# Performance work log

Hardware: AMD Instinct MI355X
Metric: run time of the kernel (lower is better)

Reference implementation:

```python
import jax, jax.numpy as jnp
import numpy as np

N, C, H, W = 512, 2048, 16, 8
NUM_CLASSES = 751
ALPHA = 1.2      # margin
LAMB = 0.5       # self.l
SIGMA = 0.8      # osm_sigma
BN_EPS = 1e-5


def setup_inputs() -> dict:
    key = jax.random.key(0)
    k1, k2, k3 = jax.random.split(key, 3)
    features = jax.random.normal(k1, (N, C, H, W), dtype=jnp.float32)
    targets = jax.random.randint(k2, (N,), 0, NUM_CLASSES)
    gamma = jnp.ones((C,), dtype=jnp.float32)  # BN weight, init 1 (weights_init_kaiming)
    # kaiming_uniform_(a=sqrt(5)) on [NUM_CLASSES, C]: bound = 1/sqrt(C)
    bound = 1.0 / np.sqrt(C)
    weight = jax.random.uniform(k3, (NUM_CLASSES, C), jnp.float32, -bound, bound)
    return {"features": features, "targets": targets, "gamma": gamma, "weight": weight}


def _l2norm(x, axis=-1):
    return x / jnp.maximum(jnp.linalg.norm(x, axis=axis, keepdims=True), 1e-12)


def reference(features, targets, gamma, weight):
    n = features.shape[0]
    # AdaptiveAvgPool2d(1) + Flatten
    global_feat = jnp.mean(features, axis=(2, 3))  # [n, C]
    # NoBiasBatchNorm1d (training mode: batch stats, biased var, no bias)
    mu = jnp.mean(global_feat, axis=0)
    var = jnp.var(global_feat, axis=0)
    bn_feat = (global_feat - mu) / jnp.sqrt(var + BN_EPS) * gamma
    bn_feat = _l2norm(bn_feat, axis=1)  # F.normalize

    # pairwise euclidean distance
    sq = jnp.sum(bn_feat * bn_feat, axis=1)                       # [n]
    dist2 = sq[:, None] + sq[None, :] - 2.0 * (bn_feat @ bn_feat.T)
    dist = jnp.sqrt(jnp.clip(dist2, 1e-12, None))                 # [n, n]

    S_pos = jnp.exp(-(dist * dist) / (SIGMA * SIGMA))
    S_neg = jnp.clip(ALPHA - dist, 1e-12, None)
    p_mask = targets[:, None] == targets[None, :]                 # [n, n] bool
    S = jnp.where(p_mask, S_pos, S_neg)

    # per-sample attention: exp(logits)[i, t_i] / sum_j exp(logits)[i, j] == softmax
    logits = bn_feat @ _l2norm(weight, axis=1).T                  # [n, num_classes]
    probs = jax.nn.softmax(logits, axis=1)
    atten = probs[jnp.arange(n), targets]                         # [n]
    A = jnp.minimum(atten[None, :], atten[:, None])               # [n, n]

    Wmat = S * A
    off_diag = 1.0 - jnp.eye(n, dtype=Wmat.dtype)
    W_P = Wmat * p_mask.astype(Wmat.dtype) * off_diag
    W_N = Wmat * (~p_mask).astype(Wmat.dtype) * off_diag

    L_P = 0.5 * jnp.sum(W_P * dist * dist) / jnp.sum(W_P)
    L_N = 0.5 * jnp.sum(W_N * S_neg * S_neg) / jnp.sum(W_N)
    L = (1.0 - LAMB) * L_P + LAMB * L_N
    return (L, global_feat)
```

## Files before the change

kernel.cpp:

```cpp
#include <hip/hip_runtime.h>
#include <hip/hip_bf16.h>
#include <math.h>

#define N_S   512
#define C_S   2048
#define HW_S  128
#define NCLS  751
#define NCLSP 768
#define ALPHA 1.2f
#define LAMB  0.5f
#define SIGMA 0.8f
#define BN_EPS 1e-5f

typedef __attribute__((ext_vector_type(8))) short short8;
typedef __attribute__((ext_vector_type(4))) float f32x4;

__device__ __forceinline__ unsigned short f2bf(float x) {
    __hip_bfloat16 h = __float2bfloat16(x);
    return *reinterpret_cast<unsigned short*>(&h);
}

__global__ void init_accum_kernel(float* __restrict__ accum) {
    if (threadIdx.x < 4) accum[threadIdx.x] = 0.0f;
}

__global__ __launch_bounds__(256) void pool_kernel(const float* __restrict__ feat,
                                                   float* __restrict__ gf,
                                                   float* __restrict__ out_gf) {
    int tid  = blockIdx.x * 256 + threadIdx.x;
    int pair = tid >> 5;
    int lane = tid & 31;
    const float4* p = reinterpret_cast<const float4*>(feat + (size_t)pair * HW_S);
    float4 v = p[lane];
    float s = v.x + v.y + v.z + v.w;
    #pragma unroll
    for (int off = 16; off > 0; off >>= 1) s += __shfl_down(s, off, 32);
    if (lane == 0) {
        float m = s * (1.0f / HW_S);
        gf[pair]     = m;
        out_gf[pair] = m;
    }
}

__global__ __launch_bounds__(256) void meanvar_kernel(const float* __restrict__ gf,
                                                      const float* __restrict__ gamma,
                                                      float* __restrict__ mu_out,
                                                      float* __restrict__ scale_out) {
    int c = blockIdx.x * 256 + threadIdx.x;
    float sum = 0.f, sumsq = 0.f;
    for (int n = 0; n < N_S; ++n) {
        float x = gf[(size_t)n * C_S + c];
        sum += x; sumsq += x * x;
    }
    float mu  = sum * (1.0f / N_S);
    float var = sumsq * (1.0f / N_S) - mu * mu;
    mu_out[c]    = mu;
    scale_out[c] = gamma[c] / sqrtf(var + BN_EPS);
}

__global__ __launch_bounds__(256) void bnnorm_kernel(const float* __restrict__ gf,
                                                     const float* __restrict__ mu,
                                                     const float* __restrict__ scale,
                                                     unsigned short* __restrict__ bnnh,
                                                     float* __restrict__ sq) {
    int n = blockIdx.x, t = threadIdx.x;
    const float* row = gf + (size_t)n * C_S;
    float v[8];
    float ss = 0.f;
    #pragma unroll
    for (int k = 0; k < 8; ++k) {
        int c = t + k * 256;
        float x = (row[c] - mu[c]) * scale[c];
        v[k] = x; ss += x * x;
    }
    __shared__ float red[4];
    __shared__ float sinv;
    #pragma unroll
    for (int off = 32; off > 0; off >>= 1) ss += __shfl_down(ss, off, 64);
    if ((t & 63) == 0) red[t >> 6] = ss;
    __syncthreads();
    if (t == 0) {
        float tot = red[0] + red[1] + red[2] + red[3];
        float inv = 1.0f / fmaxf(sqrtf(tot), 1e-12f);
        sinv  = inv;
        sq[n] = tot * inv * inv;
    }
    __syncthreads();
    float inv = sinv;
    unsigned short* orow = bnnh + (size_t)n * C_S;
    #pragma unroll
    for (int k = 0; k < 8; ++k) orow[t + k * 256] = f2bf(v[k] * inv);
}

__global__ __launch_bounds__(256) void wnorm_kernel(const float* __restrict__ w,
                                                    unsigned short* __restrict__ wnh) {
    int kcls = blockIdx.x, t = threadIdx.x;
    unsigned short* orow = wnh + (size_t)kcls * C_S;
    if (kcls >= NCLS) {
        #pragma unroll
        for (int k = 0; k < 8; ++k) orow[t + k * 256] = 0;
        return;
    }
    const float* row = w + (size_t)kcls * C_S;
    float v[8];
    float ss = 0.f;
    #pragma unroll
    for (int k = 0; k < 8; ++k) {
        float x = row[t + k * 256];
        v[k] = x; ss += x * x;
    }
    __shared__ float red[4];
    __shared__ float sinv;
    #pragma unroll
    for (int off = 32; off > 0; off >>= 1) ss += __shfl_down(ss, off, 64);
    if ((t & 63) == 0) red[t >> 6] = ss;
    __syncthreads();
    if (t == 0) sinv = 1.0f / fmaxf(sqrtf(red[0] + red[1] + red[2] + red[3]), 1e-12f);
    __syncthreads();
    float inv = sinv;
    #pragma unroll
    for (int k = 0; k < 8; ++k) orow[t + k * 256] = f2bf(v[k] * inv);
}

__global__ __launch_bounds__(256) void mfma_gemm_nt(const unsigned short* __restrict__ Ah,
                                                    const unsigned short* __restrict__ Bh,
                                                    float* __restrict__ Cm,
                                                    int K, int ldc) {
    int wave = threadIdx.x >> 6;
    int lane = threadIdx.x & 63;
    int m0 = blockIdx.x * 64 + wave * 16;
    int n0 = blockIdx.y * 64;
    int mrow = m0 + (lane & 15);
    int kq   = (lane >> 4) * 8;
    f32x4 acc0 = {0.f,0.f,0.f,0.f}, acc1 = {0.f,0.f,0.f,0.f};
    f32x4 acc2 = {0.f,0.f,0.f,0.f}, acc3 = {0.f,0.f,0.f,0.f};
    const unsigned short* arow = Ah + (size_t)mrow * K + kq;
    const unsigned short* brow = Bh + (size_t)(n0 + (lane & 15)) * K + kq;
    for (int k = 0; k < K; k += 32) {
        short8 a  = *reinterpret_cast<const short8*>(arow + k);
        short8 b0 = *reinterpret_cast<const short8*>(brow + k);
        short8 b1 = *reinterpret_cast<const short8*>(brow + 16 * K + k);
        short8 b2 = *reinterpret_cast<const short8*>(brow + 32 * K + k);
        short8 b3 = *reinterpret_cast<const short8*>(brow + 48 * K + k);
        acc0 = __builtin_amdgcn_mfma_f32_16x16x32_bf16(a, b0, acc0, 0, 0, 0);
        acc1 = __builtin_amdgcn_mfma_f32_16x16x32_bf16(a, b1, acc1, 0, 0, 0);
        acc2 = __builtin_amdgcn_mfma_f32_16x16x32_bf16(a, b2, acc2, 0, 0, 0);
        acc3 = __builtin_amdgcn_mfma_f32_16x16x32_bf16(a, b3, acc3, 0, 0, 0);
    }
    int ccol  = lane & 15;
    int crow0 = m0 + (lane >> 4) * 4;
    #pragma unroll
    for (int r = 0; r < 4; ++r) {
        float* orow = Cm + (size_t)(crow0 + r) * ldc + n0 + ccol;
        orow[0]  = acc0[r];
        orow[16] = acc1[r];
        orow[32] = acc2[r];
        orow[48] = acc3[r];
    }
}

__global__ __launch_bounds__(256) void softmax_atten_kernel(const float* __restrict__ logits,
                                                            const int* __restrict__ targets,
                                                            float* __restrict__ atten) {
    int n = blockIdx.x, t = threadIdx.x;
    const float* row = logits + (size_t)n * NCLSP;
    __shared__ float red[4];
    __shared__ float srmax, srsum;
    float m = -1e30f;
    for (int k = t; k < NCLS; k += 256) m = fmaxf(m, row[k]);
    #pragma unroll
    for (int off = 32; off > 0; off >>= 1) m = fmaxf(m, __shfl_down(m, off, 64));
    if ((t & 63) == 0) red[t >> 6] = m;
    __syncthreads();
    if (t == 0) srmax = fmaxf(fmaxf(red[0], red[1]), fmaxf(red[2], red[3]));
    __syncthreads();
    float rm = srmax;
    float s = 0.f;
    for (int k = t; k < NCLS; k += 256) s += expf(row[k] - rm);
    #pragma unroll
    for (int off = 32; off > 0; off >>= 1) s += __shfl_down(s, off, 64);
    if ((t & 63) == 0) red[t >> 6] = s;
    __syncthreads();
    if (t == 0) {
        srsum = red[0] + red[1] + red[2] + red[3];
        atten[n] = expf(row[targets[n]] - rm) / srsum;
    }
}

__global__ __launch_bounds__(256) void pair_reduce_kernel(const float* __restrict__ G,
                                                          const float* __restrict__ sq,
                                                          const float* __restrict__ atten,
                                                          const int* __restrict__ targets,
                                                          float* __restrict__ accum) {
    float numP = 0.f, denP = 0.f, numN = 0.f, denN = 0.f;
    const float inv_sig2 = 1.0f / (SIGMA * SIGMA);
    for (int p = blockIdx.x * 256 + threadIdx.x; p < N_S * N_S; p += 256 * 256) {
        int i = p >> 9, j = p & (N_S - 1);
        if (i == j) continue;
        float d2   = fmaxf(sq[i] + sq[j] - 2.0f * G[p], 1e-12f);
        float dist = sqrtf(d2);
        float sneg = fmaxf(ALPHA - dist, 1e-12f);
        float Aij  = fminf(atten[i], atten[j]);
        if (targets[i] == targets[j]) {
            float Wm = expf(-d2 * inv_sig2) * Aij;
            numP += Wm * d2; denP += Wm;
        } else {
            float Wm = sneg * Aij;
            numN += Wm * sneg * sneg; denN += Wm;
        }
    }
    #pragma unroll
    for (int off = 32; off > 0; off >>= 1) {
        numP += __shfl_down(numP, off, 64);
        denP += __shfl_down(denP, off, 64);
        numN += __shfl_down(numN, off, 64);
        denN += __shfl_down(denN, off, 64);
    }
    __shared__ float red[4][4];
    int t = threadIdx.x;
    if ((t & 63) == 0) {
        int w = t >> 6;
        red[w][0] = numP; red[w][1] = denP; red[w][2] = numN; red[w][3] = denN;
    }
    __syncthreads();
    if (t < 4) {
        float s = red[0][t] + red[1][t] + red[2][t] + red[3][t];
        atomicAdd(&accum[t], s);
    }
}

__global__ void finalize_kernel(const float* __restrict__ accum, float* __restrict__ out) {
    float L_P = 0.5f * accum[0] / accum[1];
    float L_N = 0.5f * accum[2] / accum[3];
    out[0] = (1.0f - LAMB) * L_P + LAMB * L_N;
}

extern "C" void kernel_launch(void* const* d_in, const int* in_sizes, int n_in,
                              void* d_out, int out_size, void* d_ws, size_t ws_size,
                              hipStream_t stream) {
    const float* features = (const float*)d_in[0];
    const int*   targets  = (const int*)d_in[1];
    const float* gamma    = (const float*)d_in[2];
    const float* weight   = (const float*)d_in[3];
    float* out = (float*)d_out;

    float* ws     = (float*)d_ws;
    float* gf     = ws;
    float* mu     = gf + 1048576;
    float* scale  = mu + 2048;
    float* sq     = scale + 2048;
    float* atten  = sq + 512;
    float* accum  = atten + 512;
    float* logits = accum + 8;
    float* G      = logits + 393216;
    unsigned short* bnnh = (unsigned short*)(G + 262144);
    unsigned short* wnh  = bnnh + 1048576;

    hipLaunchKernelGGL(init_accum_kernel, dim3(1), dim3(64), 0, stream, accum);
    hipLaunchKernelGGL(pool_kernel, dim3((N_S * C_S) / 8), dim3(256), 0, stream,
                       features, gf, out + 1);
    hipLaunchKernelGGL(meanvar_kernel, dim3(C_S / 256), dim3(256), 0, stream,
                       gf, gamma, mu, scale);
    hipLaunchKernelGGL(bnnorm_kernel, dim3(N_S), dim3(256), 0, stream,
                       gf, mu, scale, bnnh, sq);
    hipLaunchKernelGGL(wnorm_kernel, dim3(NCLSP), dim3(256), 0, stream, weight, wnh);
    hipLaunchKernelGGL(mfma_gemm_nt, dim3(N_S / 64, NCLSP / 64), dim3(256), 0, stream,
                       bnnh, wnh, logits, C_S, NCLSP);
    hipLaunchKernelGGL(softmax_atten_kernel, dim3(N_S), dim3(256), 0, stream,
                       logits, targets, atten);
    hipLaunchKernelGGL(mfma_gemm_nt, dim3(N_S / 64, N_S / 64), dim3(256), 0, stream,
                       bnnh, bnnh, G, C_S, N_S);
    hipLaunchKernelGGL(pair_reduce_kernel, dim3(256), dim3(256), 0, stream,
                       G, sq, atten, targets, accum);
    hipLaunchKernelGGL(finalize_kernel, dim3(1), dim3(1), 0, stream, accum, out);
}
```

Baseline: 787.1 us.

## Restructure pooling, column stats, GEMM grid and fold init/finalize kernels

The pool kernel now handles 16 pairs per block with two float4 loads per lane, zeroes the accumulators itself, and writes pooled features straight into the output buffer, which removes the extra gf copy. meanvar now splits the 512 rows across 8 thread groups per column with a shared-memory reduction, so many more blocks run. The GEMM becomes one wave per block over 16-row tiles, which multiplies the block count for better CU occupancy, and its k loop is unrolled by two. The finalize kernel is folded into pair_reduce with a last-block-done atomic counter. This removes two launches but relies on threadfence and atomic visibility being correct.

```diff
diff --git a/kernel.cpp b/kernel.cpp
--- a/kernel.cpp
+++ b/kernel.cpp
@@ -20,42 +20,48 @@
     return *reinterpret_cast<unsigned short*>(&h);
 }
 
-__global__ void init_accum_kernel(float* __restrict__ accum) {
-    if (threadIdx.x < 4) accum[threadIdx.x] = 0.0f;
-}
-
 __global__ __launch_bounds__(256) void pool_kernel(const float* __restrict__ feat,
-                                                   float* __restrict__ gf,
-                                                   float* __restrict__ out_gf) {
-    int tid  = blockIdx.x * 256 + threadIdx.x;
-    int pair = tid >> 5;
-    int lane = tid & 31;
+                                                   float* __restrict__ out_gf,
+                                                   float* __restrict__ accum) {
+    if (blockIdx.x == 0 && threadIdx.x < 8) accum[threadIdx.x] = 0.0f;
+    int pair = blockIdx.x * 16 + (threadIdx.x >> 4);
+    int sub  = threadIdx.x & 15;
     const float4* p = reinterpret_cast<const float4*>(feat + (size_t)pair * HW_S);
-    float4 v = p[lane];
-    float s = v.x + v.y + v.z + v.w;
-    #pragma unroll
-    for (int off = 16; off > 0; off >>= 1) s += __shfl_down(s, off, 32);
-    if (lane == 0) {
-        float m = s * (1.0f / HW_S);
-        gf[pair]     = m;
-        out_gf[pair] = m;
-    }
+    float4 v0 = p[sub];
+    float4 v1 = p[sub + 16];
+    float s = (v0.x + v0.y + v0.z + v0.w) + (v1.x + v1.y + v1.z + v1.w);
+    #pragma unroll
+    for (int off = 8; off > 0; off >>= 1) s += __shfl_down(s, off, 16);
+    if (sub == 0) out_gf[pair] = s * (1.0f / HW_S);
 }
 
 __global__ __launch_bounds__(256) void meanvar_kernel(const float* __restrict__ gf,
                                                       const float* __restrict__ gamma,
                                                       float* __restrict__ mu_out,
                                                       float* __restrict__ scale_out) {
-    int c = blockIdx.x * 256 + threadIdx.x;
+    int tc = threadIdx.x & 31;
+    int tr = threadIdx.x >> 5;
+    int c  = blockIdx.x * 32 + tc;
+    const float* col = gf + c;
     float sum = 0.f, sumsq = 0.f;
-    for (int n = 0; n < N_S; ++n) {
-        float x = gf[(size_t)n * C_S + c];
+    #pragma unroll 4
+    for (int n = tr * 64; n < tr * 64 + 64; ++n) {
+        float x = col[(size_t)n * C_S];
         sum += x; sumsq += x * x;
     }
-    float mu  = sum * (1.0f / N_S);
-    float var = sumsq * (1.0f / N_S) - mu * mu;
-    mu_out[c]    = mu;
-    scale_out[c] = gamma[c] / sqrtf(var + BN_EPS);
+    __shared__ float s1[8][32], s2[8][32];
+    s1[tr][tc] = sum; s2[tr][tc] = sumsq;
+    __syncthreads();
+    if (threadIdx.x < 32) {
+        int cc = blockIdx.x * 32 + threadIdx.x;
+        float a = 0.f, b = 0.f;
+        #pragma unroll
+        for (int r = 0; r < 8; ++r) { a += s1[r][threadIdx.x]; b += s2[r][threadIdx.x]; }
+        float mu  = a * (1.0f / N_S);
+        float var = b * (1.0f / N_S) - mu * mu;
+        mu_out[cc]    = mu;
+        scale_out[cc] = gamma[cc] / sqrtf(var + BN_EPS);
+    }
 }
 
 __global__ __launch_bounds__(256) void bnnorm_kernel(const float* __restrict__ gf,
@@ -122,13 +128,12 @@
     for (int k = 0; k < 8; ++k) orow[t + k * 256] = f2bf(v[k] * inv);
 }
 
-__global__ __launch_bounds__(256) void mfma_gemm_nt(const unsigned short* __restrict__ Ah,
-                                                    const unsigned short* __restrict__ Bh,
-                                                    float* __restrict__ Cm,
-                                                    int K, int ldc) {
-    int wave = threadIdx.x >> 6;
+__global__ __launch_bounds__(64) void mfma_gemm_nt(const unsigned short* __restrict__ Ah,
+                                                   const unsigned short* __restrict__ Bh,
+                                                   float* __restrict__ Cm,
+                                                   int K, int ldc) {
     int lane = threadIdx.x & 63;
-    int m0 = blockIdx.x * 64 + wave * 16;
+    int m0 = blockIdx.x * 16;
     int n0 = blockIdx.y * 64;
     int mrow = m0 + (lane & 15);
     int kq   = (lane >> 4) * 8;
@@ -136,6 +141,7 @@
     f32x4 acc2 = {0.f,0.f,0.f,0.f}, acc3 = {0.f,0.f,0.f,0.f};
     const unsigned short* arow = Ah + (size_t)mrow * K + kq;
     const unsigned short* brow = Bh + (size_t)(n0 + (lane & 15)) * K + kq;
+    #pragma unroll 2
     for (int k = 0; k < K; k += 32) {
         short8 a  = *reinterpret_cast<const short8*>(arow + k);
         short8 b0 = *reinterpret_cast<const short8*>(brow + k);
@@ -191,7 +197,8 @@
                                                           const float* __restrict__ sq,
                                                           const float* __restrict__ atten,
                                                           const int* __restrict__ targets,
-                                                          float* __restrict__ accum) {
+                                                          float* __restrict__ accum,
+                                                          float* __restrict__ out) {
     float numP = 0.f, denP = 0.f, numN = 0.f, denN = 0.f;
     const float inv_sig2 = 1.0f / (SIGMA * SIGMA);
     for (int p = blockIdx.x * 256 + threadIdx.x; p < N_S * N_S; p += 256 * 256) {
@@ -227,12 +234,20 @@
         float s = red[0][t] + red[1][t] + red[2][t] + red[3][t];
         atomicAdd(&accum[t], s);
     }
-}
-
-__global__ void finalize_kernel(const float* __restrict__ accum, float* __restrict__ out) {
-    float L_P = 0.5f * accum[0] / accum[1];
-    float L_N = 0.5f * accum[2] / accum[3];
-    out[0] = (1.0f - LAMB) * L_P + LAMB * L_N;
+    __syncthreads();
+    if (t == 0) {
+        __threadfence();
+        unsigned prev = atomicAdd(reinterpret_cast<unsigned*>(accum + 4), 1u);
+        if (prev == gridDim.x - 1) {
+            float a0 = atomicAdd(&accum[0], 0.0f);
+            float a1 = atomicAdd(&accum[1], 0.0f);
+            float a2 = atomicAdd(&accum[2], 0.0f);
+            float a3 = atomicAdd(&accum[3], 0.0f);
+            float L_P = 0.5f * a0 / a1;
+            float L_N = 0.5f * a2 / a3;
+            out[0] = (1.0f - LAMB) * L_P + LAMB * L_N;
+        }
+    }
 }
 
 extern "C" void kernel_launch(void* const* d_in, const int* in_sizes, int n_in,
@@ -243,10 +258,10 @@
     const float* gamma    = (const float*)d_in[2];
     const float* weight   = (const float*)d_in[3];
     float* out = (float*)d_out;
+    float* gf  = out + 1;
 
     float* ws     = (float*)d_ws;
-    float* gf     = ws;
-    float* mu     = gf + 1048576;
+    float* mu     = ws;
     float* scale  = mu + 2048;
     float* sq     = scale + 2048;
     float* atten  = sq + 512;
@@ -256,21 +271,19 @@
     unsigned short* bnnh = (unsigned short*)(G + 262144);
     unsigned short* wnh  = bnnh + 1048576;
 
-    hipLaunchKernelGGL(init_accum_kernel, dim3(1), dim3(64), 0, stream, accum);
-    hipLaunchKernelGGL(pool_kernel, dim3((N_S * C_S) / 8), dim3(256), 0, stream,
-                       features, gf, out + 1);
-    hipLaunchKernelGGL(meanvar_kernel, dim3(C_S / 256), dim3(256), 0, stream,
+    hipLaunchKernelGGL(pool_kernel, dim3((N_S * C_S) / 16), dim3(256), 0, stream,
+                       features, gf, accum);
+    hipLaunchKernelGGL(meanvar_kernel, dim3(C_S / 32), dim3(256), 0, stream,
                        gf, gamma, mu, scale);
     hipLaunchKernelGGL(bnnorm_kernel, dim3(N_S), dim3(256), 0, stream,
                        gf, mu, scale, bnnh, sq);
     hipLaunchKernelGGL(wnorm_kernel, dim3(NCLSP), dim3(256), 0, stream, weight, wnh);
-    hipLaunchKernelGGL(mfma_gemm_nt, dim3(N_S / 64, NCLSP / 64), dim3(256), 0, stream,
+    hipLaunchKernelGGL(mfma_gemm_nt, dim3(N_S / 16, NCLSP / 64), dim3(64), 0, stream,
                        bnnh, wnh, logits, C_S, NCLSP);
     hipLaunchKernelGGL(softmax_atten_kernel, dim3(N_S), dim3(256), 0, stream,
                        logits, targets, atten);
-    hipLaunchKernelGGL(mfma_gemm_nt, dim3(N_S / 64, N_S / 64), dim3(256), 0, stream,
+    hipLaunchKernelGGL(mfma_gemm_nt, dim3(N_S / 16, N_S / 64), dim3(64), 0, stream,
                        bnnh, bnnh, G, C_S, N_S);
     hipLaunchKernelGGL(pair_reduce_kernel, dim3(256), dim3(256), 0, stream,
-                       G, sq, atten, targets, accum);
-    hipLaunchKernelGGL(finalize_kernel, dim3(1), dim3(1), 0, stream, accum, out);
-}
+                       G, sq, atten, targets, accum, out);
+}
```

Measured after the change: 746.9 us. 5.1% less time.
